# Kernel optimization log

Measured on AMD Instinct MI355X. Metric: run time of the kernel, lower is better.

## Reference

```python
import jax, jax.numpy as jnp
import numpy as np
import math

N_HEAD = 16


def setup_inputs() -> dict:
    key = jax.random.key(0)
    ks = jax.random.split(key, 5)
    B, T, C = 2, 2048, 2048
    x = jax.random.normal(ks[0], (B, T, C), dtype=jnp.float32)
    # additive causal mask: 0 on/below diagonal, large negative above
    causal = jnp.tril(jnp.ones((T, T), dtype=bool))
    attention_mask = jnp.where(causal, 0.0, -1e9).astype(jnp.float32)[None, None]
    scale = 0.02
    W_attn = jax.random.normal(ks[1], (C, 3 * C), dtype=jnp.float32) * scale
    b_attn = jax.random.normal(ks[2], (3 * C,), dtype=jnp.float32) * scale
    W_proj = jax.random.normal(ks[3], (C, C), dtype=jnp.float32) * scale
    b_proj = jax.random.normal(ks[4], (C,), dtype=jnp.float32) * scale
    return {"x": x, "attention_mask": attention_mask, "W_attn": W_attn,
            "b_attn": b_attn, "W_proj": W_proj, "b_proj": b_proj}


def reference(x, attention_mask, W_attn, b_attn, W_proj, b_proj):
    B, T, C = x.shape
    H = N_HEAD
    Dh = C // H
    qkv = x @ W_attn + b_attn                      # [B,T,3C]
    q, k, v = jnp.split(qkv, 3, axis=2)            # each [B,T,C]
    current_cache = jnp.concatenate([k, v], axis=2)  # [B,T,2C]
    qh = q.reshape(B, T, H, Dh).transpose(0, 2, 1, 3)  # [B,H,T,Dh]
    kh = k.reshape(B, T, H, Dh).transpose(0, 2, 1, 3)
    vh = v.reshape(B, T, H, Dh).transpose(0, 2, 1, 3)
    att = jnp.einsum('bhqd,bhkd->bhqk', qh, kh) * (1.0 / math.sqrt(Dh))
    att = att + attention_mask                     # broadcast [1,1,T,T]
    att = jax.nn.softmax(att, axis=-1)
    y = jnp.einsum('bhqk,bhkd->bhqd', att, vh)     # [B,H,T,Dh]
    y = y.transpose(0, 2, 1, 3).reshape(B, T, C)
    y = y @ W_proj + b_proj                        # [B,T,C]
    return (y, current_cache)
```

## Files before the change

kernel.cpp:

```cpp
#include <hip/hip_runtime.h>

typedef __attribute__((ext_vector_type(8))) short bf16x8;
typedef __attribute__((ext_vector_type(4))) float f32x4;

#define MFMA16(a, b, c) __builtin_amdgcn_mfma_f32_16x16x32_bf16((a), (b), (c), 0, 0, 0)

static __device__ __forceinline__ short f2bf(float f) {
  unsigned u = __builtin_bit_cast(unsigned, f);
  unsigned r = (u + 0x7FFFu + ((u >> 16) & 1u)) >> 16;
  return (short)(unsigned short)r;
}
static __device__ __forceinline__ unsigned pack2(float lo, float hi) {
  return (unsigned)(unsigned short)f2bf(lo) | ((unsigned)(unsigned short)f2bf(hi) << 16);
}

static __device__ __forceinline__ void glds16(const void* g, void* l) {
  __builtin_amdgcn_global_load_lds((const __attribute__((address_space(1))) unsigned*)g,
                                   (__attribute__((address_space(3))) unsigned*)l, 16, 0, 0);
}

__global__ __launch_bounds__(256) void cvt_bf16_kernel(const float* __restrict__ in,
                                                       short* __restrict__ out) {
  size_t i = ((size_t)blockIdx.x * 256 + threadIdx.x) * 8;
  float4 a = *(const float4*)(in + i);
  float4 b = *(const float4*)(in + i + 4);
  uint4 o;
  o.x = pack2(a.x, a.y);
  o.y = pack2(a.z, a.w);
  o.z = pack2(b.x, b.y);
  o.w = pack2(b.z, b.w);
  *(uint4*)(out + i) = o;
}

__global__ __launch_bounds__(256) void transpose_cvt_kernel(const float* __restrict__ in,
                                                            short* __restrict__ out, int R,
                                                            int Cc) {
  __shared__ float tile[64][65];
  int tx = threadIdx.x & 15, ty = threadIdx.x >> 4;
  int r0 = blockIdx.y * 64, c0 = blockIdx.x * 64;
#pragma unroll
  for (int i = 0; i < 4; i++) {
    int r = ty + i * 16;
    float4 v = *(const float4*)(in + (size_t)(r0 + r) * Cc + c0 + tx * 4);
    tile[r][tx * 4 + 0] = v.x;
    tile[r][tx * 4 + 1] = v.y;
    tile[r][tx * 4 + 2] = v.z;
    tile[r][tx * 4 + 3] = v.w;
  }
  __syncthreads();
#pragma unroll
  for (int i = 0; i < 4; i++) {
    int co = ty + i * 16;
    uint2 o;
    o.x = pack2(tile[tx * 4 + 0][co], tile[tx * 4 + 1][co]);
    o.y = pack2(tile[tx * 4 + 2][co], tile[tx * 4 + 3][co]);
    *(uint2*)(out + (size_t)(c0 + co) * R + r0 + tx * 4) = o;
  }
}

__global__ __launch_bounds__(256) void gemm_qkv_kernel(const short* __restrict__ A,
                                                       const short* __restrict__ Bt,
                                                       const float* __restrict__ bias,
                                                       short* __restrict__ q_bf,
                                                       short* __restrict__ k_bf,
                                                       short* __restrict__ v_bf,
                                                       float* __restrict__ cache) {
  const int K = 2048;
  __shared__ __align__(16) short As[128 * 32];
  __shared__ __align__(16) short Bs[128 * 32];
  int tid = threadIdx.x;
  int lane = tid & 63, wid = tid >> 6;
  int wr = wid >> 1, wc = wid & 1;
  int l15 = lane & 15, l4 = lane >> 4;
  int rowBase = blockIdx.y * 128, colBase = blockIdx.x * 128;

  int srow = lane >> 2;
  int schunk = ((lane & 3) ^ ((lane >> 3) & 3)) * 8;
  int g0 = wid * 16, g1 = 64 + wid * 16;
  const short* Ag0 = A + (size_t)(rowBase + g0 + srow) * K + schunk;
  const short* Ag1 = A + (size_t)(rowBase + g1 + srow) * K + schunk;
  const short* Bg0 = Bt + (size_t)(colBase + g0 + srow) * K + schunk;
  const short* Bg1 = Bt + (size_t)(colBase + g1 + srow) * K + schunk;
  short* la0 = &As[g0 * 32];
  short* la1 = &As[g1 * 32];
  short* lb0 = &Bs[g0 * 32];
  short* lb1 = &Bs[g1 * 32];

  int fchunk = (l4 ^ ((l15 >> 1) & 3)) * 8;

  f32x4 zero = {0.f, 0.f, 0.f, 0.f};
  f32x4 acc[4][4];
#pragma unroll
  for (int i = 0; i < 4; i++)
#pragma unroll
    for (int j = 0; j < 4; j++) acc[i][j] = zero;

  for (int k0 = 0; k0 < K; k0 += 32) {
    __syncthreads();
    glds16(Ag0 + k0, la0);
    glds16(Ag1 + k0, la1);
    glds16(Bg0 + k0, lb0);
    glds16(Bg1 + k0, lb1);
    __syncthreads();
    bf16x8 af[4], bfv[4];
#pragma unroll
    for (int mt = 0; mt < 4; mt++)
      af[mt] = *(const bf16x8*)&As[(wr * 64 + mt * 16 + l15) * 32 + fchunk];
#pragma unroll
    for (int nt = 0; nt < 4; nt++)
      bfv[nt] = *(const bf16x8*)&Bs[(wc * 64 + nt * 16 + l15) * 32 + fchunk];
#pragma unroll
    for (int mt = 0; mt < 4; mt++)
#pragma unroll
      for (int nt = 0; nt < 4; nt++) acc[mt][nt] = MFMA16(af[mt], bfv[nt], acc[mt][nt]);
  }

#pragma unroll
  for (int mt = 0; mt < 4; mt++) {
#pragma unroll
    for (int nt = 0; nt < 4; nt++) {
      int col = colBase + wc * 64 + nt * 16 + l15;
      float bv = bias[col];
#pragma unroll
      for (int r = 0; r < 4; r++) {
        int row = rowBase + wr * 64 + mt * 16 + l4 * 4 + r;
        float v = acc[mt][nt][r] + bv;
        int bb = row >> 11, t = row & 2047;
        if (col < 2048) {
          q_bf[(size_t)row * 2048 + col] = f2bf(v * 0.08838834764831845f);
        } else if (col < 4096) {
          int cc = col - 2048;
          k_bf[(size_t)row * 2048 + cc] = f2bf(v);
          cache[(size_t)(bb * 2048 + t) * 4096 + cc] = v;
        } else {
          int vc = col - 4096;
          cache[(size_t)(bb * 2048 + t) * 4096 + 2048 + vc] = v;
          v_bf[(size_t)row * 2048 + vc] = f2bf(v);
        }
      }
    }
  }
}

__global__ __launch_bounds__(256) void vpost_kernel(const short* __restrict__ vb,
                                                    short* __restrict__ vt) {
  __shared__ short tile[64][72];
  int tid = threadIdx.x;
  int z = blockIdx.z;
  int b = z >> 4, hh = z & 15;
  int t0 = blockIdx.x * 64, d0 = blockIdx.y * 64;
  int tx = tid & 7, ty = tid >> 3;
#pragma unroll
  for (int i = 0; i < 2; i++) {
    int r = ty + i * 32;
    *(uint4*)&tile[r][tx * 8] =
        *(const uint4*)(vb + (size_t)(b * 2048 + t0 + r) * 2048 + hh * 128 + d0 + tx * 8);
  }
  __syncthreads();
#pragma unroll
  for (int i = 0; i < 2; i++) {
    int dr = ty + i * 32;
    short tmp[8];
#pragma unroll
    for (int j = 0; j < 8; j++) {
      int p = tx * 8 + j;
      int tl = (p & 32) + ((p & 1) << 4) + ((p >> 1) & 15);
      tmp[j] = tile[tl][dr];
    }
    *(uint4*)(vt + (size_t)(z * 128 + d0 + dr) * 2048 + t0 + tx * 8) = *(uint4*)tmp;
  }
}

#define LDT 40
__global__ __launch_bounds__(256) void gemm_proj_kernel(const short* __restrict__ A,
                                                        const short* __restrict__ Bt,
                                                        const float* __restrict__ bias,
                                                        float* __restrict__ out_y) {
  const int K = 2048;
  __shared__ short As[64 * LDT];
  __shared__ short Bs[128 * LDT];
  int tid = threadIdx.x;
  int lane = tid & 63, wid = tid >> 6;
  int wr = wid >> 1, wc = wid & 1;
  int l15 = lane & 15, l4 = lane >> 4;
  int rowBase = blockIdx.y * 64, colBase = blockIdx.x * 128;
  int srow = tid >> 2, skc = (tid & 3) * 8;

  f32x4 zero = {0.f, 0.f, 0.f, 0.f};
  f32x4 acc[2][4];
#pragma unroll
  for (int i = 0; i < 2; i++)
#pragma unroll
    for (int j = 0; j < 4; j++) acc[i][j] = zero;

  const short* Ap0 = A + (size_t)(rowBase + srow) * K + skc;
  const short* Bp0 = Bt + (size_t)(colBase + srow) * K + skc;
  const short* Bp1 = Bt + (size_t)(colBase + srow + 64) * K + skc;

  for (int k0 = 0; k0 < K; k0 += 32) {
    uint4 a0 = *(const uint4*)(Ap0 + k0);
    uint4 b0 = *(const uint4*)(Bp0 + k0);
    uint4 b1 = *(const uint4*)(Bp1 + k0);
    __syncthreads();
    *(uint4*)&As[srow * LDT + skc] = a0;
    *(uint4*)&Bs[srow * LDT + skc] = b0;
    *(uint4*)&Bs[(srow + 64) * LDT + skc] = b1;
    __syncthreads();
    bf16x8 af[2], bfv[4];
#pragma unroll
    for (int mt = 0; mt < 2; mt++)
      af[mt] = *(const bf16x8*)&As[(wr * 32 + mt * 16 + l15) * LDT + l4 * 8];
#pragma unroll
    for (int nt = 0; nt < 4; nt++)
      bfv[nt] = *(const bf16x8*)&Bs[(wc * 64 + nt * 16 + l15) * LDT + l4 * 8];
#pragma unroll
    for (int mt = 0; mt < 2; mt++)
#pragma unroll
      for (int nt = 0; nt < 4; nt++) acc[mt][nt] = MFMA16(af[mt], bfv[nt], acc[mt][nt]);
  }

#pragma unroll
  for (int mt = 0; mt < 2; mt++) {
#pragma unroll
    for (int nt = 0; nt < 4; nt++) {
      int col = colBase + wc * 64 + nt * 16 + l15;
      float bv = bias[col];
#pragma unroll
      for (int r = 0; r < 4; r++) {
        int row = rowBase + wr * 32 + mt * 16 + l4 * 4 + r;
        out_y[(size_t)row * 2048 + col] = acc[mt][nt][r] + bv;
      }
    }
  }
}

#define LDK 136
#define LDV 72
#define LDP 72

__global__ __launch_bounds__(512, 4) void attn_kernel(const short* __restrict__ qb,
                                                      const short* __restrict__ kb,
                                                      const short* __restrict__ vtb,
                                                      short* __restrict__ attout) {
  __shared__ short Ks[64 * LDK];
  __shared__ short Vs[128 * LDV];
  __shared__ short Ps[8][16 * LDP];

  int tid = threadIdx.x;
  int lane = tid & 63, wid = tid >> 6;
  int l15 = lane & 15, l4 = lane >> 4;
  int qlo = blockIdx.x, qhi = 31 - qlo;
  int h = blockIdx.y, b = blockIdx.z;
  int myqt = (wid < 4) ? qhi : qlo;
  int qrow0 = myqt * 64 + (wid & 3) * 16;
  size_t qkbase = (size_t)b * 2048 * 2048 + (size_t)h * 128;
  size_t vbase = (size_t)((b * 16 + h) * 128) * 2048;

  bf16x8 qf[4];
#pragma unroll
  for (int kk = 0; kk < 4; kk++)
    qf[kk] = *(const bf16x8*)(qb + qkbase + (size_t)(qrow0 + l15) * 2048 + kk * 32 + l4 * 8);

  short onev = (short)0x3F80;
  bf16x8 ones = {onev, onev, onev, onev, onev, onev, onev, onev};

  f32x4 zero = {0.f, 0.f, 0.f, 0.f};
  f32x4 o[8], ol;
#pragma unroll
  for (int n = 0; n < 8; n++) o[n] = zero;
  ol = zero;

  for (int kt = 0; kt <= qhi; kt++) {
    int kt0 = kt * 64;
    __syncthreads();
#pragma unroll
    for (int i = 0; i < 2; i++) {
      int c = i * 512 + tid;
      int kr = c >> 4, kc = (c & 15) * 8;
      *(uint4*)&Ks[kr * LDK + kc] = *(const uint4*)(kb + qkbase + (size_t)(kt0 + kr) * 2048 + kc);
    }
#pragma unroll
    for (int i = 0; i < 2; i++) {
      int c = i * 512 + tid;
      int dr = c >> 3, tc = (c & 7) * 8;
      *(uint4*)&Vs[dr * LDV + tc] = *(const uint4*)(vtb + vbase + (size_t)dr * 2048 + kt0 + tc);
    }
    __syncthreads();

    if (wid < 4 || kt <= qlo) {
      f32x4 s[4];
#pragma unroll
      for (int nt = 0; nt < 4; nt++) s[nt] = zero;
#pragma unroll
      for (int kk = 0; kk < 4; kk++) {
#pragma unroll
        for (int nt = 0; nt < 4; nt++) {
          bf16x8 kf = *(const bf16x8*)&Ks[(nt * 16 + l15) * LDK + kk * 32 + l4 * 8];
          s[nt] = MFMA16(qf[kk], kf, s[nt]);
        }
      }

      if (kt == myqt) {
#pragma unroll
        for (int nt = 0; nt < 4; nt++) {
          int colg = kt0 + nt * 16 + l15;
#pragma unroll
          for (int r = 0; r < 4; r++) {
            int rowg = qrow0 + l4 * 4 + r;
            if (colg > rowg) s[nt][r] = -1e30f;
          }
        }
      }

#pragma unroll
      for (int r = 0; r < 4; r++) {
        float p0 = __expf(s[0][r]);
        float p1 = __expf(s[1][r]);
        float p2 = __expf(s[2][r]);
        float p3 = __expf(s[3][r]);
        int prow = (l4 * 4 + r) * LDP;
        *(unsigned*)&Ps[wid][prow + 2 * l15] = pack2(p0, p1);
        *(unsigned*)&Ps[wid][prow + 32 + 2 * l15] = pack2(p2, p3);
      }

#pragma unroll
      for (int kk = 0; kk < 2; kk++) {
        bf16x8 pf = *(const bf16x8*)&Ps[wid][l15 * LDP + kk * 32 + l4 * 8];
        ol = MFMA16(pf, ones, ol);
#pragma unroll
        for (int n = 0; n < 8; n++) {
          bf16x8 vf = *(const bf16x8*)&Vs[(n * 16 + l15) * LDV + kk * 32 + l4 * 8];
          o[n] = MFMA16(pf, vf, o[n]);
        }
      }
    }
  }

  float rl[4];
#pragma unroll
  for (int r = 0; r < 4; r++) rl[r] = 1.0f / ol[r];
#pragma unroll
  for (int n = 0; n < 8; n++)
#pragma unroll
    for (int r = 0; r < 4; r++)
      attout[qkbase + (size_t)(qrow0 + l4 * 4 + r) * 2048 + n * 16 + l15] =
          f2bf(o[n][r] * rl[r]);
}

extern "C" void kernel_launch(void* const* d_in, const int* in_sizes, int n_in, void* d_out,
                              int out_size, void* d_ws, size_t ws_size, hipStream_t stream) {
  const float* x = (const float*)d_in[0];
  const float* W_attn = (const float*)d_in[2];
  const float* b_attn = (const float*)d_in[3];
  const float* W_proj = (const float*)d_in[4];
  const float* b_proj = (const float*)d_in[5];
  float* y = (float*)d_out;
  float* cache = y + (size_t)4096 * 2048;

  char* p = (char*)d_ws;
  short* x_bf = (short*)p;   p += (size_t)8388608 * 2;
  short* q_bf = (short*)p;   p += (size_t)8388608 * 2;
  short* k_bf = (short*)p;   p += (size_t)8388608 * 2;
  short* vt_bf = (short*)p;  p += (size_t)8388608 * 2;
  short* att_bf = (short*)p; p += (size_t)8388608 * 2;
  short* wt_attn = (short*)p; p += (size_t)12582912 * 2;
  short* wt_proj = (short*)p; p += (size_t)4194304 * 2;
  short* v_bf = att_bf;

  cvt_bf16_kernel<<<4096, 256, 0, stream>>>(x, x_bf);
  transpose_cvt_kernel<<<dim3(96, 32), 256, 0, stream>>>(W_attn, wt_attn, 2048, 6144);
  transpose_cvt_kernel<<<dim3(32, 32), 256, 0, stream>>>(W_proj, wt_proj, 2048, 2048);
  gemm_qkv_kernel<<<dim3(48, 32), 256, 0, stream>>>(x_bf, wt_attn, b_attn, q_bf, k_bf, v_bf,
                                                    cache);
  vpost_kernel<<<dim3(32, 2, 32), 256, 0, stream>>>(v_bf, vt_bf);
  attn_kernel<<<dim3(16, 16, 2), 512, 0, stream>>>(q_bf, k_bf, vt_bf, att_bf);
  gemm_proj_kernel<<<dim3(16, 64), 256, 0, stream>>>(att_bf, wt_proj, b_proj, y);
}
```

Baseline: 485.8 us.

## Stage QKV epilogue through LDS and enlarge proj GEMM tile with direct-to-LDS loads

```diff
diff --git a/kernel.cpp b/kernel.cpp
--- a/kernel.cpp
+++ b/kernel.cpp
@@ -66,8 +66,9 @@
                                                        short* __restrict__ v_bf,
                                                        float* __restrict__ cache) {
   const int K = 2048;
-  __shared__ __align__(16) short As[128 * 32];
-  __shared__ __align__(16) short Bs[128 * 32];
+  __shared__ __align__(16) short smem[128 * 64];
+  short* As = smem;
+  short* Bs = smem + 128 * 32;
   int tid = threadIdx.x;
   int lane = tid & 63, wid = tid >> 6;
   int wr = wid >> 1, wc = wid & 1;
@@ -115,30 +116,52 @@
       for (int nt = 0; nt < 4; nt++) acc[mt][nt] = MFMA16(af[mt], bfv[nt], acc[mt][nt]);
   }
 
-#pragma unroll
-  for (int mt = 0; mt < 4; mt++) {
-#pragma unroll
-    for (int nt = 0; nt < 4; nt++) {
-      int col = colBase + wc * 64 + nt * 16 + l15;
-      float bv = bias[col];
-#pragma unroll
-      for (int r = 0; r < 4; r++) {
-        int row = rowBase + wr * 64 + mt * 16 + l4 * 4 + r;
-        float v = acc[mt][nt][r] + bv;
-        int bb = row >> 11, t = row & 2047;
-        if (col < 2048) {
-          q_bf[(size_t)row * 2048 + col] = f2bf(v * 0.08838834764831845f);
-        } else if (col < 4096) {
-          int cc = col - 2048;
-          k_bf[(size_t)row * 2048 + cc] = f2bf(v);
-          cache[(size_t)(bb * 2048 + t) * 4096 + cc] = v;
-        } else {
-          int vc = col - 4096;
-          cache[(size_t)(bb * 2048 + t) * 4096 + 2048 + vc] = v;
-          v_bf[(size_t)row * 2048 + vc] = f2bf(v);
+  int seg = colBase >> 11;
+  int colLoc = colBase & 2047;
+  float scale = (seg == 0) ? 0.08838834764831845f : 1.0f;
+  short* outp = (seg == 0) ? q_bf : (seg == 1) ? k_bf : v_bf;
+  short(*Cs)[64] = (short(*)[64])smem;
+
+  float bv[4];
+#pragma unroll
+  for (int nt = 0; nt < 4; nt++) bv[nt] = bias[colBase + wc * 64 + nt * 16 + l15];
+
+#pragma unroll
+  for (int p = 0; p < 2; p++) {
+    __syncthreads();
+    if (wc == p) {
+#pragma unroll
+      for (int mt = 0; mt < 4; mt++)
+#pragma unroll
+        for (int nt = 0; nt < 4; nt++)
+#pragma unroll
+          for (int r = 0; r < 4; r++)
+            Cs[wr * 64 + mt * 16 + l4 * 4 + r][nt * 16 + l15] =
+                f2bf((acc[mt][nt][r] + bv[nt]) * scale);
+    }
+    __syncthreads();
+#pragma unroll
+    for (int q = 0; q < 4; q++) {
+      int row = q * 32 + (tid >> 3);
+      int c8 = (tid & 7) * 8;
+      *(uint4*)(outp + (size_t)(rowBase + row) * 2048 + colLoc + p * 64 + c8) =
+          *(const uint4*)&Cs[row][c8];
+    }
+  }
+
+  if (seg) {
+    int coff = (seg == 1) ? 0 : 2048;
+#pragma unroll
+    for (int mt = 0; mt < 4; mt++)
+#pragma unroll
+      for (int nt = 0; nt < 4; nt++) {
+        int cc = coff + colLoc + wc * 64 + nt * 16 + l15;
+#pragma unroll
+        for (int r = 0; r < 4; r++) {
+          int row = rowBase + wr * 64 + mt * 16 + l4 * 4 + r;
+          cache[(size_t)row * 4096 + cc] = acc[mt][nt][r] + bv[nt];
         }
       }
-    }
   }
 }
 
@@ -171,64 +194,70 @@
   }
 }
 
-#define LDT 40
 __global__ __launch_bounds__(256) void gemm_proj_kernel(const short* __restrict__ A,
                                                         const short* __restrict__ Bt,
                                                         const float* __restrict__ bias,
                                                         float* __restrict__ out_y) {
   const int K = 2048;
-  __shared__ short As[64 * LDT];
-  __shared__ short Bs[128 * LDT];
+  __shared__ __align__(16) short As[128 * 32];
+  __shared__ __align__(16) short Bs[128 * 32];
   int tid = threadIdx.x;
   int lane = tid & 63, wid = tid >> 6;
   int wr = wid >> 1, wc = wid & 1;
   int l15 = lane & 15, l4 = lane >> 4;
-  int rowBase = blockIdx.y * 64, colBase = blockIdx.x * 128;
-  int srow = tid >> 2, skc = (tid & 3) * 8;
+  int rowBase = blockIdx.y * 128, colBase = blockIdx.x * 128;
+
+  int srow = lane >> 2;
+  int schunk = ((lane & 3) ^ ((lane >> 3) & 3)) * 8;
+  int g0 = wid * 16, g1 = 64 + wid * 16;
+  const short* Ag0 = A + (size_t)(rowBase + g0 + srow) * K + schunk;
+  const short* Ag1 = A + (size_t)(rowBase + g1 + srow) * K + schunk;
+  const short* Bg0 = Bt + (size_t)(colBase + g0 + srow) * K + schunk;
+  const short* Bg1 = Bt + (size_t)(colBase + g1 + srow) * K + schunk;
+  short* la0 = &As[g0 * 32];
+  short* la1 = &As[g1 * 32];
+  short* lb0 = &Bs[g0 * 32];
+  short* lb1 = &Bs[g1 * 32];
+
+  int fchunk = (l4 ^ ((l15 >> 1) & 3)) * 8;
 
   f32x4 zero = {0.f, 0.f, 0.f, 0.f};
-  f32x4 acc[2][4];
-#pragma unroll
-  for (int i = 0; i < 2; i++)
+  f32x4 acc[4][4];
+#pragma unroll
+  for (int i = 0; i < 4; i++)
 #pragma unroll
     for (int j = 0; j < 4; j++) acc[i][j] = zero;
 
-  const short* Ap0 = A + (size_t)(rowBase + srow) * K + skc;
-  const short* Bp0 = Bt + (size_t)(colBase + srow) * K + skc;
-  const short* Bp1 = Bt + (size_t)(colBase + srow + 64) * K + skc;
-
   for (int k0 = 0; k0 < K; k0 += 32) {
-    uint4 a0 = *(const uint4*)(Ap0 + k0);
-    uint4 b0 = *(const uint4*)(Bp0 + k0);
-    uint4 b1 = *(const uint4*)(Bp1 + k0);
-    __syncthreads();
-    *(uint4*)&As[srow * LDT + skc] = a0;
-    *(uint4*)&Bs[srow * LDT + skc] = b0;
-    *(uint4*)&Bs[(srow + 64) * LDT + skc] = b1;
-    __syncthreads();
-    bf16x8 af[2], bfv[4];
-#pragma unroll
-    for (int mt = 0; mt < 2; mt++)
-      af[mt] = *(const bf16x8*)&As[(wr * 32 + mt * 16 + l15) * LDT + l4 * 8];
+    __syncthreads();
+    glds16(Ag0 + k0, la0);
+    glds16(Ag1 + k0, la1);
+    glds16(Bg0 + k0, lb0);
+    glds16(Bg1 + k0, lb1);
+    __syncthreads();
+    bf16x8 af[4], bfv[4];
+#pragma unroll
+    for (int mt = 0; mt < 4; mt++)
+      af[mt] = *(const bf16x8*)&As[(wr * 64 + mt * 16 + l15) * 32 + fchunk];
 #pragma unroll
     for (int nt = 0; nt < 4; nt++)
-      bfv[nt] = *(const bf16x8*)&Bs[(wc * 64 + nt * 16 + l15) * LDT + l4 * 8];
-#pragma unroll
-    for (int mt = 0; mt < 2; mt++)
+      bfv[nt] = *(const bf16x8*)&Bs[(wc * 64 + nt * 16 + l15) * 32 + fchunk];
+#pragma unroll
+    for (int mt = 0; mt < 4; mt++)
 #pragma unroll
       for (int nt = 0; nt < 4; nt++) acc[mt][nt] = MFMA16(af[mt], bfv[nt], acc[mt][nt]);
   }
 
 #pragma unroll
-  for (int mt = 0; mt < 2; mt++) {
+  for (int mt = 0; mt < 4; mt++) {
 #pragma unroll
     for (int nt = 0; nt < 4; nt++) {
       int col = colBase + wc * 64 + nt * 16 + l15;
-      float bv = bias[col];
+      float bvv = bias[col];
 #pragma unroll
       for (int r = 0; r < 4; r++) {
-        int row = rowBase + wr * 32 + mt * 16 + l4 * 4 + r;
-        out_y[(size_t)row * 2048 + col] = acc[mt][nt][r] + bv;
+        int row = rowBase + wr * 64 + mt * 16 + l4 * 4 + r;
+        out_y[(size_t)row * 2048 + col] = acc[mt][nt][r] + bvv;
       }
     }
   }
@@ -374,5 +403,5 @@
                                                     cache);
   vpost_kernel<<<dim3(32, 2, 32), 256, 0, stream>>>(v_bf, vt_bf);
   attn_kernel<<<dim3(16, 16, 2), 512, 0, stream>>>(q_bf, k_bf, vt_bf, att_bf);
-  gemm_proj_kernel<<<dim3(16, 64), 256, 0, stream>>>(att_bf, wt_proj, b_proj, y);
-}
+  gemm_proj_kernel<<<dim3(16, 32), 256, 0, stream>>>(att_bf, wt_proj, b_proj, y);
+}
```

Result: faster. 460.2 us (-5.3%).
